# Performance work log

Hardware: AMD Instinct MI355X
Metric: run time of the kernel (lower is better)

The kernel has to match this reference:

```python
import jax, jax.numpy as jnp
import numpy as np

C_SIZE = 512
DOWN = 8
W = C_SIZE // DOWN           # 64
REG = 10.0
N_ITER = 100                 # num_of_iter_in_ot

COOD = jnp.arange(0, C_SIZE, DOWN, dtype=jnp.float32) + DOWN / 2.0  # (W,)


def _cost_matrix(pts):
    # pts: (N,2) pixel coords -> squared L2 distance to every grid cell, (N, W*W)
    x = pts[:, 0:1]
    y = pts[:, 1:2]
    cood = COOD[None, :]
    x_dis = -2.0 * x * cood + x * x + cood * cood      # (N, W)
    y_dis = -2.0 * y * cood + y * y + cood * cood      # (N, W)
    dis = y_dis[:, :, None] + x_dis[:, None, :]        # (N, W, W): rows=y, cols=x
    return dis.reshape(pts.shape[0], -1)


def _asgd_semi_dual(a, b, M, idxs):
    # POT ot.stochastic.solve_semi_dual_entropic with method='asgd'.
    # a: (n,) target (point) weights; b: (m,) source (density) weights; M: (n, m).
    n, m = M.shape
    lr = 1.0 / jnp.max(a / REG)          # POT default lr
    log_b = jnp.log(b)

    def step(carry, xk):
        cur, ave = carry
        i, k = xk
        Mi = M[i]
        khi = jax.nn.softmax((cur - Mi) / REG + log_b)   # stable softmax
        cur = cur + (lr / jnp.sqrt(k)) * (b - khi)
        ave = cur / k + (1.0 - 1.0 / k) * ave
        return (cur, ave), None

    ks = jnp.arange(1, idxs.shape[0] + 1, dtype=jnp.float32)
    (_, beta), _ = jax.lax.scan(step, (jnp.zeros(m, M.dtype), jnp.zeros(m, M.dtype)), (idxs, ks))
    # c-transform: alpha_i = -reg * log sum_j exp((beta_j - M_ij)/reg) * b_j
    alpha = -REG * jax.scipy.special.logsumexp((beta[None, :] - M) / REG + log_b[None, :], axis=1)
    pi = jnp.exp((alpha[:, None] + beta[None, :] - M) / REG) * a[:, None] * b[None, :]
    return beta, pi


def _per_sample(normed, unnormed, pts, idxs):
    # normed, unnormed: (W, W); pts: (N, 2); idxs: (N_ITER,)
    n = pts.shape[0]
    a = jnp.full((n,), 1.0 / n, dtype=jnp.float32)
    dis = jax.lax.stop_gradient(_cost_matrix(pts))            # cupy path: no grad
    b = jax.lax.stop_gradient(normed.reshape(-1))             # src_prob detached
    beta, pi = _asgd_semi_dual(a, b, dis, idxs)
    beta = jax.lax.stop_gradient(beta)
    ot_obj = jnp.sum(normed.reshape(-1) * beta)
    src = jax.lax.stop_gradient(unnormed.reshape(-1))         # source_density detached
    sc = src.sum()
    denom = sc * sc + 1e-16
    im_grad = jax.lax.stop_gradient(sc / denom * beta - jnp.sum(src * beta) / denom)
    loss = jnp.sum(unnormed.reshape(-1) * im_grad)
    wd = jnp.sum(dis * jax.lax.stop_gradient(pi))
    return loss, wd, ot_obj


def setup_inputs() -> dict:
    key = jax.random.key(0)
    k1, k2 = jax.random.split(key, 2)
    unnormed = jax.random.uniform(k1, (16, 1, W, W), dtype=jnp.float32)
    normed = unnormed / unnormed.sum(axis=(1, 2, 3), keepdims=True)
    points = jax.random.uniform(k2, (16, 512, 2), dtype=jnp.float32) * C_SIZE
    return {"normed_density": normed, "unnormed_density": unnormed, "points": points}


def reference(normed_density, unnormed_density, points):
    B = normed_density.shape[0]
    # random coordinate indices for ASGD (constant, deterministic)
    idxs = jax.random.randint(jax.random.key(1), (B, N_ITER), 0, points.shape[1])
    loss, wd, ot_obj = jax.vmap(_per_sample)(
        normed_density[:, 0], unnormed_density[:, 0], points, idxs)
    return jnp.stack([loss.sum(), wd.sum(), ot_obj.sum()])
```

## Files before the change

kernel.cpp:

```cpp
#include <hip/hip_runtime.h>
#include <math.h>

#define NSAMP 16
#define NPTS  512
#define MDIM  4096
#define NIT   100

#define R0MAX 48


__device__ __forceinline__ int swz(int r, int c) {
  return r * 64 + (c ^ ((r & 1) << 4));
}

__device__ __forceinline__ void tf2x32(unsigned k0, unsigned k1,
                                       unsigned c0, unsigned c1,
                                       unsigned &o0, unsigned &o1)
{
  unsigned ks2 = k0 ^ k1 ^ 0x1BD11BDAu;
  unsigned x0 = c0 + k0, x1 = c1 + k1;
#define ROT(r) x0 += x1; x1 = (x1 << (r)) | (x1 >> (32 - (r))); x1 ^= x0;
#define G0 ROT(13) ROT(15) ROT(26) ROT(6)
#define G1 ROT(17) ROT(29) ROT(16) ROT(24)
  G0 x0 += k1;  x1 += ks2 + 1u;
  G1 x0 += ks2; x1 += k0  + 2u;
  G0 x0 += k0;  x1 += k1  + 3u;
  G1 x0 += k1;  x1 += ks2 + 4u;
  G0 x0 += ks2; x1 += k0  + 5u;
#undef G0
#undef G1
#undef ROT
  o0 = x0; o1 = x1;
}

__device__ __forceinline__ int rand_idx(int f)
{
  unsigned ka, kb, w0, w1;
  tf2x32(0u, 1u, 0u, 1u, ka, kb);
  tf2x32(ka, kb, 0u, (unsigned)f, w0, w1);
  return (int)((w0 ^ w1) & 511u);
}

template<int CTRL>
__device__ __forceinline__ float dpp_mv(float v, float id)
{
  return __int_as_float(__builtin_amdgcn_update_dpp(
      __float_as_int(id), __float_as_int(v), CTRL, 0xF, 0xF, false));
}

__device__ __forceinline__ float waveSum(float v)
{
  v += dpp_mv<0x111>(v, 0.0f);
  v += dpp_mv<0x112>(v, 0.0f);
  v += dpp_mv<0x114>(v, 0.0f);
  v += dpp_mv<0x118>(v, 0.0f);
  v += dpp_mv<0x142>(v, 0.0f);
  v += dpp_mv<0x143>(v, 0.0f);
  return __int_as_float(__builtin_amdgcn_readlane(__float_as_int(v), 63));
}

__global__ __launch_bounds__(1024) void kern_scan(
    const float *__restrict__ normed, const float *__restrict__ pts,
    float *__restrict__ out, float *__restrict__ wglob)
{
  const int s = blockIdx.x;
  const int t = threadIdx.x;
  const int v = t >> 6;
  const int L = t & 63;

  __shared__ float2 dav[MDIM];
  __shared__ float  barr[MDIM];
  __shared__ float4 cstA[NIT + 4];
  __shared__ int2   cstB[NIT + 4];
  __shared__ float  spfin;
  __shared__ float  otred[16];

  #pragma unroll
  for (int l = 0; l < 4; ++l) {
    const int r = 4 * v + l;
    const float bv = normed[s * MDIM + r * 64 + L];
    const int idx = swz(r, L);
    dav[idx]  = make_float2(__logf(bv), 0.0f);
    barr[idx] = bv;
  }
  if (t < NIT + 4) {
    const int kk = t < NIT ? t : (NIT - 1);
    const int idx = rand_idx(s * NIT + kk);
    const float2 p = ((const float2 *)pts)[s * NPTS + idx];
    const int rn = (int)floorf((p.y - 4.0f) * 0.125f + 0.5f);
    const int cn = (int)floorf((p.x - 4.0f) * 0.125f + 0.5f);
    int r0 = rn - 7; r0 = r0 < 0 ? 0 : (r0 > R0MAX ? R0MAX : r0);
    int c0 = cn - 7; c0 = c0 < 0 ? 0 : (c0 > R0MAX ? R0MAX : c0);
    const float kf    = (float)(kk + 1);
    const float step1 = 512.0f * __builtin_amdgcn_rsqf(kf);
    const float Pk    = step1 * (0.01f * (101.0f - kf));
    cstA[t] = make_float4(p.x - (float)(8 * c0 + 4),
                          p.y - (float)(8 * r0 + 4), step1, Pk);
    cstB[t] = make_int2(r0, c0);
  }
  __syncthreads();

  const int rbase = L >> 4;
  const int cbase = L & 15;
  const float fc8 = (float)(8 * cbase);
  const float fr8 = (float)(8 * rbase);

  if (t == 64) {
    float SPa = 0.0f;
    for (int k = 0; k < NIT; ++k) SPa += cstA[k].w;
    spfin = SPa;
  }
  if (v == 0) {
    float A = 0.0f;
    float4 cA = cstA[0];
    int2   cB = cstB[0];
    int j0 = swz(cB.x + rbase, cB.y + cbase);
    float2 c0v = dav[j0      ]; float b0v = barr[j0      ];
    float2 c1v = dav[j0 + 256]; float b1v = barr[j0 + 256];
    float2 c2v = dav[j0 + 512]; float b2v = barr[j0 + 512];
    float2 c3v = dav[j0 + 768]; float b3v = barr[j0 + 768];

    for (int k = 0; k < NIT; ++k) {
      const float4 cAn = cstA[k + 1];
      const int2   cBn = cstB[k + 1];

      const float dx  = cA.x - fc8;
      const float dxx = dx * dx;
      const float ty  = cA.y - fr8;
      const float e0 = __expf(fmaf(fmaf(ty,          ty,          dxx), -0.1f, fmaf(b0v, A, c0v.x)));
      const float e1 = __expf(fmaf(fmaf(ty - 32.0f, ty - 32.0f, dxx), -0.1f, fmaf(b1v, A, c1v.x)));
      const float e2 = __expf(fmaf(fmaf(ty - 64.0f, ty - 64.0f, dxx), -0.1f, fmaf(b2v, A, c2v.x)));
      const float e3 = __expf(fmaf(fmaf(ty - 96.0f, ty - 96.0f, dxx), -0.1f, fmaf(b3v, A, c3v.x)));

      const float S    = waveSum((e0 + e1) + (e2 + e3));
      const float invS = __builtin_amdgcn_rcpf(S);
      const float cD = cA.z * invS, cAv = cA.w * invS;

      c0v.x = fmaf(-cD, e0, c0v.x); c0v.y = fmaf(cAv, e0, c0v.y);
      c1v.x = fmaf(-cD, e1, c1v.x); c1v.y = fmaf(cAv, e1, c1v.y);
      c2v.x = fmaf(-cD, e2, c2v.x); c2v.y = fmaf(cAv, e2, c2v.y);
      c3v.x = fmaf(-cD, e3, c3v.x); c3v.y = fmaf(cAv, e3, c3v.y);
      dav[j0      ] = c0v;
      dav[j0 + 256] = c1v;
      dav[j0 + 512] = c2v;
      dav[j0 + 768] = c3v;

      A += cA.z;

      cA = cAn; cB = cBn;
      j0 = swz(cB.x + rbase, cB.y + cbase);
      c0v = dav[j0      ]; b0v = barr[j0      ];
      c1v = dav[j0 + 256]; b1v = barr[j0 + 256];
      c2v = dav[j0 + 512]; b2v = barr[j0 + 512];
      c3v = dav[j0 + 768]; b3v = barr[j0 + 768];
    }
  }
  __syncthreads();

  {
    const float SP = spfin;
    float p_ot = 0.0f;
    #pragma unroll
    for (int l = 0; l < 4; ++l) {
      const int r   = 4 * v + l;
      const int idx = swz(r, L);
      const float2 cd = dav[idx];
      const float bb  = barr[idx];
      const float tt  = fmaf(bb, SP, -cd.y);
      wglob[s * MDIM + r * 64 + L] = tt + __logf(bb);
      p_ot = fmaf(bb, 10.0f * tt, p_ot);
    }
    p_ot = waveSum(p_ot);
    if (L == 0) otred[v] = p_ot;
  }
  __syncthreads();
  if (t == 0) {
    float ot = 0.0f;
    #pragma unroll
    for (int i = 0; i < 16; ++i) ot += otred[i];
    atomicAdd(&out[2], ot);
  }
}

__global__ __launch_bounds__(1024) void kern_wd(
    const float *__restrict__ pts, const float *__restrict__ wglob,
    float *__restrict__ out)
{
  const int s = blockIdx.x >> 3;
  const int q = blockIdx.x & 7;
  const int t = threadIdx.x;
  const int v = t >> 6;
  const int L = t & 63;

  __shared__ float  wlds[MDIM];
  __shared__ float2 pts2[64];
  __shared__ float  wdred[16];

  #pragma unroll
  for (int l = 0; l < 4; ++l) {
    const int r = 4 * v + l;
    wlds[swz(r, L)] = wglob[s * MDIM + r * 64 + L];
  }
  if (t < 64) pts2[t] = ((const float2 *)pts)[s * NPTS + 64 * q + t];
  __syncthreads();

  const int rbase = L >> 4;
  const int cbase = L & 15;

  float pe[4], pq[4];
  #pragma unroll
  for (int i = 0; i < 4; ++i) {
    const int p = 4 * v + i;
    const float2 pt = pts2[p];
    const float x = pt.x, y = pt.y;
    const int rn = (int)floorf((y - 4.0f) * 0.125f + 0.5f);
    const int cn = (int)floorf((x - 4.0f) * 0.125f + 0.5f);
    int r0 = rn - 7; r0 = r0 < 0 ? 0 : (r0 > R0MAX ? R0MAX : r0);
    int c0 = cn - 7; c0 = c0 < 0 ? 0 : (c0 > R0MAX ? R0MAX : c0);
    const int rl = r0 + rbase;
    const int cl = c0 + cbase;
    const int j0 = swz(rl, cl);

    const float dx  = x - (float)(8 * cl + 4);
    const float dxx = dx * dx;
    const float ty  = y - (float)(8 * rl + 4);
    float spe = 0.0f, spq = 0.0f;
    #pragma unroll
    for (int qq4 = 0; qq4 < 4; ++qq4) {
      const float wv = wlds[j0 + 256 * qq4];
      const float dy = ty - (float)(32 * qq4);
      const float qq = fmaf(dy, dy, dxx);
      const float e  = __expf(fmaf(qq, -0.1f, wv));
      spe += e;
      spq = fmaf(e, qq, spq);
    }
    pe[i] = spe; pq[i] = spq;
  }
  #pragma unroll
  for (int i = 0; i < 4; ++i) { pe[i] += dpp_mv<0x111>(pe[i], 0.0f); pq[i] += dpp_mv<0x111>(pq[i], 0.0f); }
  #pragma unroll
  for (int i = 0; i < 4; ++i) { pe[i] += dpp_mv<0x112>(pe[i], 0.0f); pq[i] += dpp_mv<0x112>(pq[i], 0.0f); }
  #pragma unroll
  for (int i = 0; i < 4; ++i) { pe[i] += dpp_mv<0x114>(pe[i], 0.0f); pq[i] += dpp_mv<0x114>(pq[i], 0.0f); }
  #pragma unroll
  for (int i = 0; i < 4; ++i) { pe[i] += dpp_mv<0x118>(pe[i], 0.0f); pq[i] += dpp_mv<0x118>(pq[i], 0.0f); }
  #pragma unroll
  for (int i = 0; i < 4; ++i) { pe[i] += dpp_mv<0x142>(pe[i], 0.0f); pq[i] += dpp_mv<0x142>(pq[i], 0.0f); }
  #pragma unroll
  for (int i = 0; i < 4; ++i) { pe[i] += dpp_mv<0x143>(pe[i], 0.0f); pq[i] += dpp_mv<0x143>(pq[i], 0.0f); }

  float wdacc = 0.0f;
  #pragma unroll
  for (int i = 0; i < 4; ++i) {
    const float PE = __int_as_float(__builtin_amdgcn_readlane(__float_as_int(pe[i]), 63));
    const float PQ = __int_as_float(__builtin_amdgcn_readlane(__float_as_int(pq[i]), 63));
    wdacc = fmaf(PQ, __builtin_amdgcn_rcpf(PE), wdacc);
  }
  if (L == 0) wdred[v] = wdacc;
  __syncthreads();
  if (t == 0) {
    float wd = 0.0f;
    #pragma unroll
    for (int i = 0; i < 16; ++i) wd += wdred[i];
    atomicAdd(&out[1], wd * (1.0f / 512.0f));
  }
}

extern "C" void kernel_launch(void* const* d_in, const int* in_sizes, int n_in,
                              void* d_out, int out_size, void* d_ws, size_t ws_size,
                              hipStream_t stream)
{
  (void)in_sizes; (void)n_in; (void)out_size; (void)ws_size;
  const float *normed = (const float *)d_in[0];
  const float *pts    = (const float *)d_in[2];
  float *out   = (float *)d_out;
  float *wglob = (float *)d_ws;

  hipMemsetAsync(out, 0, 3 * sizeof(float), stream);
  kern_scan<<<dim3(NSAMP),     dim3(1024), 0, stream>>>(normed, pts, out, wglob);
  kern_wd  <<<dim3(NSAMP * 8), dim3(1024), 0, stream>>>(pts, wglob, out);
}
```

Before: 84.30 us.

## Fuse scan and WD kernels into one launch with per-sample flag handoff

Merges the two kernels into a single launch. The first 16 blocks run the ASGD scan and publish their per-sample result through a release flag in the workspace. The remaining 128 blocks spin on an acquire load of that flag, then compute the transport cost. This removes a kernel launch and the gap between kernels, but adds a flag memset and spin-waiting. It also relies on the producer blocks being scheduled alongside the consumers, which is normally safe here with 144 blocks on a large GPU.

New measurement: 119.8 us. 42.1% more time.

```diff
diff --git a/kernel.cpp b/kernel.cpp
--- a/kernel.cpp
+++ b/kernel.cpp
@@ -59,210 +59,214 @@
   return __int_as_float(__builtin_amdgcn_readlane(__float_as_int(v), 63));
 }
 
-__global__ __launch_bounds__(1024) void kern_scan(
+__global__ __launch_bounds__(1024) void kern_all(
     const float *__restrict__ normed, const float *__restrict__ pts,
-    float *__restrict__ out, float *__restrict__ wglob)
-{
-  const int s = blockIdx.x;
+    float *__restrict__ out, float *__restrict__ wglob,
+    unsigned *__restrict__ flags)
+{
   const int t = threadIdx.x;
   const int v = t >> 6;
   const int L = t & 63;
+  const int rbase = L >> 4;
+  const int cbase = L & 15;
 
   __shared__ float2 dav[MDIM];
   __shared__ float  barr[MDIM];
   __shared__ float4 cstA[NIT + 4];
   __shared__ int2   cstB[NIT + 4];
   __shared__ float  spfin;
-  __shared__ float  otred[16];
-
-  #pragma unroll
-  for (int l = 0; l < 4; ++l) {
-    const int r = 4 * v + l;
-    const float bv = normed[s * MDIM + r * 64 + L];
-    const int idx = swz(r, L);
-    dav[idx]  = make_float2(__logf(bv), 0.0f);
-    barr[idx] = bv;
-  }
-  if (t < NIT + 4) {
-    const int kk = t < NIT ? t : (NIT - 1);
-    const int idx = rand_idx(s * NIT + kk);
-    const float2 p = ((const float2 *)pts)[s * NPTS + idx];
-    const int rn = (int)floorf((p.y - 4.0f) * 0.125f + 0.5f);
-    const int cn = (int)floorf((p.x - 4.0f) * 0.125f + 0.5f);
-    int r0 = rn - 7; r0 = r0 < 0 ? 0 : (r0 > R0MAX ? R0MAX : r0);
-    int c0 = cn - 7; c0 = c0 < 0 ? 0 : (c0 > R0MAX ? R0MAX : c0);
-    const float kf    = (float)(kk + 1);
-    const float step1 = 512.0f * __builtin_amdgcn_rsqf(kf);
-    const float Pk    = step1 * (0.01f * (101.0f - kf));
-    cstA[t] = make_float4(p.x - (float)(8 * c0 + 4),
-                          p.y - (float)(8 * r0 + 4), step1, Pk);
-    cstB[t] = make_int2(r0, c0);
-  }
-  __syncthreads();
-
-  const int rbase = L >> 4;
-  const int cbase = L & 15;
-  const float fc8 = (float)(8 * cbase);
-  const float fr8 = (float)(8 * rbase);
-
-  if (t == 64) {
-    float SPa = 0.0f;
-    for (int k = 0; k < NIT; ++k) SPa += cstA[k].w;
-    spfin = SPa;
-  }
-  if (v == 0) {
-    float A = 0.0f;
-    float4 cA = cstA[0];
-    int2   cB = cstB[0];
-    int j0 = swz(cB.x + rbase, cB.y + cbase);
-    float2 c0v = dav[j0      ]; float b0v = barr[j0      ];
-    float2 c1v = dav[j0 + 256]; float b1v = barr[j0 + 256];
-    float2 c2v = dav[j0 + 512]; float b2v = barr[j0 + 512];
-    float2 c3v = dav[j0 + 768]; float b3v = barr[j0 + 768];
-
-    for (int k = 0; k < NIT; ++k) {
-      const float4 cAn = cstA[k + 1];
-      const int2   cBn = cstB[k + 1];
-
-      const float dx  = cA.x - fc8;
+  __shared__ float2 pts2[64];
+  __shared__ float  red[16];
+
+  if (blockIdx.x < NSAMP) {
+    const int s = blockIdx.x;
+
+    #pragma unroll
+    for (int l = 0; l < 4; ++l) {
+      const int r = 4 * v + l;
+      const float bv = normed[s * MDIM + r * 64 + L];
+      const int idx = swz(r, L);
+      dav[idx]  = make_float2(__logf(bv), 0.0f);
+      barr[idx] = bv;
+    }
+    if (t < NIT + 4) {
+      const int kk = t < NIT ? t : (NIT - 1);
+      const int idx = rand_idx(s * NIT + kk);
+      const float2 p = ((const float2 *)pts)[s * NPTS + idx];
+      const int rn = (int)floorf((p.y - 4.0f) * 0.125f + 0.5f);
+      const int cn = (int)floorf((p.x - 4.0f) * 0.125f + 0.5f);
+      int r0 = rn - 7; r0 = r0 < 0 ? 0 : (r0 > R0MAX ? R0MAX : r0);
+      int c0 = cn - 7; c0 = c0 < 0 ? 0 : (c0 > R0MAX ? R0MAX : c0);
+      const float kf    = (float)(kk + 1);
+      const float step1 = 512.0f * __builtin_amdgcn_rsqf(kf);
+      const float Pk    = step1 * (0.01f * (101.0f - kf));
+      cstA[t] = make_float4(p.x - (float)(8 * c0 + 4),
+                            p.y - (float)(8 * r0 + 4), step1, Pk);
+      cstB[t] = make_int2(r0, c0);
+    }
+    __syncthreads();
+
+    const float fc8 = (float)(8 * cbase);
+    const float fr8 = (float)(8 * rbase);
+
+    if (t == 64) {
+      float SPa = 0.0f;
+      for (int k = 0; k < NIT; ++k) SPa += cstA[k].w;
+      spfin = SPa;
+    }
+    if (v == 0) {
+      float A = 0.0f;
+      float4 cA = cstA[0];
+      int2   cB = cstB[0];
+      int j0 = swz(cB.x + rbase, cB.y + cbase);
+      float2 c0v = dav[j0      ]; float b0v = barr[j0      ];
+      float2 c1v = dav[j0 + 256]; float b1v = barr[j0 + 256];
+      float2 c2v = dav[j0 + 512]; float b2v = barr[j0 + 512];
+      float2 c3v = dav[j0 + 768]; float b3v = barr[j0 + 768];
+
+      for (int k = 0; k < NIT; ++k) {
+        const float4 cAn = cstA[k + 1];
+        const int2   cBn = cstB[k + 1];
+
+        const float dx  = cA.x - fc8;
+        const float dxx = dx * dx;
+        const float ty  = cA.y - fr8;
+        const float e0 = __expf(fmaf(fmaf(ty,          ty,          dxx), -0.1f, fmaf(b0v, A, c0v.x)));
+        const float e1 = __expf(fmaf(fmaf(ty - 32.0f, ty - 32.0f, dxx), -0.1f, fmaf(b1v, A, c1v.x)));
+        const float e2 = __expf(fmaf(fmaf(ty - 64.0f, ty - 64.0f, dxx), -0.1f, fmaf(b2v, A, c2v.x)));
+        const float e3 = __expf(fmaf(fmaf(ty - 96.0f, ty - 96.0f, dxx), -0.1f, fmaf(b3v, A, c3v.x)));
+
+        const float S    = waveSum((e0 + e1) + (e2 + e3));
+        const float invS = __builtin_amdgcn_rcpf(S);
+        const float cD = cA.z * invS, cAv = cA.w * invS;
+
+        c0v.x = fmaf(-cD, e0, c0v.x); c0v.y = fmaf(cAv, e0, c0v.y);
+        c1v.x = fmaf(-cD, e1, c1v.x); c1v.y = fmaf(cAv, e1, c1v.y);
+        c2v.x = fmaf(-cD, e2, c2v.x); c2v.y = fmaf(cAv, e2, c2v.y);
+        c3v.x = fmaf(-cD, e3, c3v.x); c3v.y = fmaf(cAv, e3, c3v.y);
+        dav[j0      ] = c0v;
+        dav[j0 + 256] = c1v;
+        dav[j0 + 512] = c2v;
+        dav[j0 + 768] = c3v;
+
+        A += cA.z;
+
+        cA = cAn; cB = cBn;
+        j0 = swz(cB.x + rbase, cB.y + cbase);
+        c0v = dav[j0      ]; b0v = barr[j0      ];
+        c1v = dav[j0 + 256]; b1v = barr[j0 + 256];
+        c2v = dav[j0 + 512]; b2v = barr[j0 + 512];
+        c3v = dav[j0 + 768]; b3v = barr[j0 + 768];
+      }
+    }
+    __syncthreads();
+
+    {
+      const float SP = spfin;
+      float p_ot = 0.0f;
+      #pragma unroll
+      for (int l = 0; l < 4; ++l) {
+        const int r   = 4 * v + l;
+        const int idx = swz(r, L);
+        const float2 cd = dav[idx];
+        const float bb  = barr[idx];
+        const float tt  = fmaf(bb, SP, -cd.y);
+        wglob[s * MDIM + r * 64 + L] = tt + __logf(bb);
+        p_ot = fmaf(bb, 10.0f * tt, p_ot);
+      }
+      p_ot = waveSum(p_ot);
+      if (L == 0) red[v] = p_ot;
+    }
+    __syncthreads();
+    if (t == 0) {
+      float ot = 0.0f;
+      #pragma unroll
+      for (int i = 0; i < 16; ++i) ot += red[i];
+      atomicAdd(&out[2], ot);
+      __threadfence();
+      __hip_atomic_store(&flags[s], 1u, __ATOMIC_RELEASE,
+                         __HIP_MEMORY_SCOPE_AGENT);
+    }
+  } else {
+    const int cb = blockIdx.x - NSAMP;
+    const int s = cb >> 3;
+    const int q = cb & 7;
+
+    if (t < 64) pts2[t] = ((const float2 *)pts)[s * NPTS + 64 * q + t];
+
+    if (t == 0) {
+      while (__hip_atomic_load(&flags[s], __ATOMIC_ACQUIRE,
+                               __HIP_MEMORY_SCOPE_AGENT) == 0u) {
+        __builtin_amdgcn_s_sleep(8);
+      }
+    }
+    __syncthreads();
+    __threadfence();
+
+    #pragma unroll
+    for (int l = 0; l < 4; ++l) {
+      const int r = 4 * v + l;
+      barr[swz(r, L)] = wglob[s * MDIM + r * 64 + L];
+    }
+    __syncthreads();
+
+    float pe[4], pq[4];
+    #pragma unroll
+    for (int i = 0; i < 4; ++i) {
+      const int p = 4 * v + i;
+      const float2 pt = pts2[p];
+      const float x = pt.x, y = pt.y;
+      const int rn = (int)floorf((y - 4.0f) * 0.125f + 0.5f);
+      const int cn = (int)floorf((x - 4.0f) * 0.125f + 0.5f);
+      int r0 = rn - 7; r0 = r0 < 0 ? 0 : (r0 > R0MAX ? R0MAX : r0);
+      int c0 = cn - 7; c0 = c0 < 0 ? 0 : (c0 > R0MAX ? R0MAX : c0);
+      const int rl = r0 + rbase;
+      const int cl = c0 + cbase;
+      const int j0 = swz(rl, cl);
+
+      const float dx  = x - (float)(8 * cl + 4);
       const float dxx = dx * dx;
-      const float ty  = cA.y - fr8;
-      const float e0 = __expf(fmaf(fmaf(ty,          ty,          dxx), -0.1f, fmaf(b0v, A, c0v.x)));
-      const float e1 = __expf(fmaf(fmaf(ty - 32.0f, ty - 32.0f, dxx), -0.1f, fmaf(b1v, A, c1v.x)));
-      const float e2 = __expf(fmaf(fmaf(ty - 64.0f, ty - 64.0f, dxx), -0.1f, fmaf(b2v, A, c2v.x)));
-      const float e3 = __expf(fmaf(fmaf(ty - 96.0f, ty - 96.0f, dxx), -0.1f, fmaf(b3v, A, c3v.x)));
-
-      const float S    = waveSum((e0 + e1) + (e2 + e3));
-      const float invS = __builtin_amdgcn_rcpf(S);
-      const float cD = cA.z * invS, cAv = cA.w * invS;
-
-      c0v.x = fmaf(-cD, e0, c0v.x); c0v.y = fmaf(cAv, e0, c0v.y);
-      c1v.x = fmaf(-cD, e1, c1v.x); c1v.y = fmaf(cAv, e1, c1v.y);
-      c2v.x = fmaf(-cD, e2, c2v.x); c2v.y = fmaf(cAv, e2, c2v.y);
-      c3v.x = fmaf(-cD, e3, c3v.x); c3v.y = fmaf(cAv, e3, c3v.y);
-      dav[j0      ] = c0v;
-      dav[j0 + 256] = c1v;
-      dav[j0 + 512] = c2v;
-      dav[j0 + 768] = c3v;
-
-      A += cA.z;
-
-      cA = cAn; cB = cBn;
-      j0 = swz(cB.x + rbase, cB.y + cbase);
-      c0v = dav[j0      ]; b0v = barr[j0      ];
-      c1v = dav[j0 + 256]; b1v = barr[j0 + 256];
-      c2v = dav[j0 + 512]; b2v = barr[j0 + 512];
-      c3v = dav[j0 + 768]; b3v = barr[j0 + 768];
-    }
-  }
-  __syncthreads();
-
-  {
-    const float SP = spfin;
-    float p_ot = 0.0f;
-    #pragma unroll
-    for (int l = 0; l < 4; ++l) {
-      const int r   = 4 * v + l;
-      const int idx = swz(r, L);
-      const float2 cd = dav[idx];
-      const float bb  = barr[idx];
-      const float tt  = fmaf(bb, SP, -cd.y);
-      wglob[s * MDIM + r * 64 + L] = tt + __logf(bb);
-      p_ot = fmaf(bb, 10.0f * tt, p_ot);
-    }
-    p_ot = waveSum(p_ot);
-    if (L == 0) otred[v] = p_ot;
-  }
-  __syncthreads();
-  if (t == 0) {
-    float ot = 0.0f;
-    #pragma unroll
-    for (int i = 0; i < 16; ++i) ot += otred[i];
-    atomicAdd(&out[2], ot);
-  }
-}
-
-__global__ __launch_bounds__(1024) void kern_wd(
-    const float *__restrict__ pts, const float *__restrict__ wglob,
-    float *__restrict__ out)
-{
-  const int s = blockIdx.x >> 3;
-  const int q = blockIdx.x & 7;
-  const int t = threadIdx.x;
-  const int v = t >> 6;
-  const int L = t & 63;
-
-  __shared__ float  wlds[MDIM];
-  __shared__ float2 pts2[64];
-  __shared__ float  wdred[16];
-
-  #pragma unroll
-  for (int l = 0; l < 4; ++l) {
-    const int r = 4 * v + l;
-    wlds[swz(r, L)] = wglob[s * MDIM + r * 64 + L];
-  }
-  if (t < 64) pts2[t] = ((const float2 *)pts)[s * NPTS + 64 * q + t];
-  __syncthreads();
-
-  const int rbase = L >> 4;
-  const int cbase = L & 15;
-
-  float pe[4], pq[4];
-  #pragma unroll
-  for (int i = 0; i < 4; ++i) {
-    const int p = 4 * v + i;
-    const float2 pt = pts2[p];
-    const float x = pt.x, y = pt.y;
-    const int rn = (int)floorf((y - 4.0f) * 0.125f + 0.5f);
-    const int cn = (int)floorf((x - 4.0f) * 0.125f + 0.5f);
-    int r0 = rn - 7; r0 = r0 < 0 ? 0 : (r0 > R0MAX ? R0MAX : r0);
-    int c0 = cn - 7; c0 = c0 < 0 ? 0 : (c0 > R0MAX ? R0MAX : c0);
-    const int rl = r0 + rbase;
-    const int cl = c0 + cbase;
-    const int j0 = swz(rl, cl);
-
-    const float dx  = x - (float)(8 * cl + 4);
-    const float dxx = dx * dx;
-    const float ty  = y - (float)(8 * rl + 4);
-    float spe = 0.0f, spq = 0.0f;
-    #pragma unroll
-    for (int qq4 = 0; qq4 < 4; ++qq4) {
-      const float wv = wlds[j0 + 256 * qq4];
-      const float dy = ty - (float)(32 * qq4);
-      const float qq = fmaf(dy, dy, dxx);
-      const float e  = __expf(fmaf(qq, -0.1f, wv));
-      spe += e;
-      spq = fmaf(e, qq, spq);
-    }
-    pe[i] = spe; pq[i] = spq;
-  }
-  #pragma unroll
-  for (int i = 0; i < 4; ++i) { pe[i] += dpp_mv<0x111>(pe[i], 0.0f); pq[i] += dpp_mv<0x111>(pq[i], 0.0f); }
-  #pragma unroll
-  for (int i = 0; i < 4; ++i) { pe[i] += dpp_mv<0x112>(pe[i], 0.0f); pq[i] += dpp_mv<0x112>(pq[i], 0.0f); }
-  #pragma unroll
-  for (int i = 0; i < 4; ++i) { pe[i] += dpp_mv<0x114>(pe[i], 0.0f); pq[i] += dpp_mv<0x114>(pq[i], 0.0f); }
-  #pragma unroll
-  for (int i = 0; i < 4; ++i) { pe[i] += dpp_mv<0x118>(pe[i], 0.0f); pq[i] += dpp_mv<0x118>(pq[i], 0.0f); }
-  #pragma unroll
-  for (int i = 0; i < 4; ++i) { pe[i] += dpp_mv<0x142>(pe[i], 0.0f); pq[i] += dpp_mv<0x142>(pq[i], 0.0f); }
-  #pragma unroll
-  for (int i = 0; i < 4; ++i) { pe[i] += dpp_mv<0x143>(pe[i], 0.0f); pq[i] += dpp_mv<0x143>(pq[i], 0.0f); }
-
-  float wdacc = 0.0f;
-  #pragma unroll
-  for (int i = 0; i < 4; ++i) {
-    const float PE = __int_as_float(__builtin_amdgcn_readlane(__float_as_int(pe[i]), 63));
-    const float PQ = __int_as_float(__builtin_amdgcn_readlane(__float_as_int(pq[i]), 63));
-    wdacc = fmaf(PQ, __builtin_amdgcn_rcpf(PE), wdacc);
-  }
-  if (L == 0) wdred[v] = wdacc;
-  __syncthreads();
-  if (t == 0) {
-    float wd = 0.0f;
-    #pragma unroll
-    for (int i = 0; i < 16; ++i) wd += wdred[i];
-    atomicAdd(&out[1], wd * (1.0f / 512.0f));
+      const float ty  = y - (float)(8 * rl + 4);
+      float spe = 0.0f, spq = 0.0f;
+      #pragma unroll
+      for (int qq4 = 0; qq4 < 4; ++qq4) {
+        const float wv = barr[j0 + 256 * qq4];
+        const float dy = ty - (float)(32 * qq4);
+        const float qq = fmaf(dy, dy, dxx);
+        const float e  = __expf(fmaf(qq, -0.1f, wv));
+        spe += e;
+        spq = fmaf(e, qq, spq);
+      }
+      pe[i] = spe; pq[i] = spq;
+    }
+    #pragma unroll
+    for (int i = 0; i < 4; ++i) { pe[i] += dpp_mv<0x111>(pe[i], 0.0f); pq[i] += dpp_mv<0x111>(pq[i], 0.0f); }
+    #pragma unroll
+    for (int i = 0; i < 4; ++i) { pe[i] += dpp_mv<0x112>(pe[i], 0.0f); pq[i] += dpp_mv<0x112>(pq[i], 0.0f); }
+    #pragma unroll
+    for (int i = 0; i < 4; ++i) { pe[i] += dpp_mv<0x114>(pe[i], 0.0f); pq[i] += dpp_mv<0x114>(pq[i], 0.0f); }
+    #pragma unroll
+    for (int i = 0; i < 4; ++i) { pe[i] += dpp_mv<0x118>(pe[i], 0.0f); pq[i] += dpp_mv<0x118>(pq[i], 0.0f); }
+    #pragma unroll
+    for (int i = 0; i < 4; ++i) { pe[i] += dpp_mv<0x142>(pe[i], 0.0f); pq[i] += dpp_mv<0x142>(pq[i], 0.0f); }
+    #pragma unroll
+    for (int i = 0; i < 4; ++i) { pe[i] += dpp_mv<0x143>(pe[i], 0.0f); pq[i] += dpp_mv<0x143>(pq[i], 0.0f); }
+
+    float wdacc = 0.0f;
+    #pragma unroll
+    for (int i = 0; i < 4; ++i) {
+      const float PE = __int_as_float(__builtin_amdgcn_readlane(__float_as_int(pe[i]), 63));
+      const float PQ = __int_as_float(__builtin_amdgcn_readlane(__float_as_int(pq[i]), 63));
+      wdacc = fmaf(PQ, __builtin_amdgcn_rcpf(PE), wdacc);
+    }
+    if (L == 0) red[v] = wdacc;
+    __syncthreads();
+    if (t == 0) {
+      float wd = 0.0f;
+      #pragma unroll
+      for (int i = 0; i < 16; ++i) wd += red[i];
+      atomicAdd(&out[1], wd * (1.0f / 512.0f));
+    }
   }
 }
 
@@ -273,10 +277,12 @@
   (void)in_sizes; (void)n_in; (void)out_size; (void)ws_size;
   const float *normed = (const float *)d_in[0];
   const float *pts    = (const float *)d_in[2];
-  float *out   = (float *)d_out;
-  float *wglob = (float *)d_ws;
+  float *out      = (float *)d_out;
+  float *wglob    = (float *)d_ws;
+  unsigned *flags = (unsigned *)((char *)d_ws + NSAMP * MDIM * sizeof(float));
 
   hipMemsetAsync(out, 0, 3 * sizeof(float), stream);
-  kern_scan<<<dim3(NSAMP),     dim3(1024), 0, stream>>>(normed, pts, out, wglob);
-  kern_wd  <<<dim3(NSAMP * 8), dim3(1024), 0, stream>>>(pts, wglob, out);
-}
+  hipMemsetAsync(flags, 0, NSAMP * sizeof(unsigned), stream);
+  kern_all<<<dim3(NSAMP + NSAMP * 8), dim3(1024), 0, stream>>>(
+      normed, pts, out, wglob, flags);
+}
```

## Process two ASGD iterations together when their windows do not overlap

Applied to the files above, without the earlier changes.

The serial ASGD scan loop now handles iterations in pairs. When the two sampled points' local windows in the cost grid do not overlap (checked uniformly per wave), both softmax updates are computed independently and their wave reductions are interleaved, which halves the serial chain of DPP reductions. Overlapping pairs fall back to running the two steps one after the other. This adds register pressure and branching, and relies on the windowed update touching only a bounded region.

Result: slower. 86.14 us (+2.2%).

```diff
diff --git a/kernel.cpp b/kernel.cpp
--- a/kernel.cpp
+++ b/kernel.cpp
@@ -59,6 +59,18 @@
   return __int_as_float(__builtin_amdgcn_readlane(__float_as_int(v), 63));
 }
 
+__device__ __forceinline__ void waveSum2(float &a, float &b)
+{
+  a += dpp_mv<0x111>(a, 0.0f); b += dpp_mv<0x111>(b, 0.0f);
+  a += dpp_mv<0x112>(a, 0.0f); b += dpp_mv<0x112>(b, 0.0f);
+  a += dpp_mv<0x114>(a, 0.0f); b += dpp_mv<0x114>(b, 0.0f);
+  a += dpp_mv<0x118>(a, 0.0f); b += dpp_mv<0x118>(b, 0.0f);
+  a += dpp_mv<0x142>(a, 0.0f); b += dpp_mv<0x142>(b, 0.0f);
+  a += dpp_mv<0x143>(a, 0.0f); b += dpp_mv<0x143>(b, 0.0f);
+  a = __int_as_float(__builtin_amdgcn_readlane(__float_as_int(a), 63));
+  b = __int_as_float(__builtin_amdgcn_readlane(__float_as_int(b), 63));
+}
+
 __global__ __launch_bounds__(1024) void kern_scan(
     const float *__restrict__ normed, const float *__restrict__ pts,
     float *__restrict__ out, float *__restrict__ wglob)
@@ -112,47 +124,120 @@
   }
   if (v == 0) {
     float A = 0.0f;
-    float4 cA = cstA[0];
-    int2   cB = cstB[0];
-    int j0 = swz(cB.x + rbase, cB.y + cbase);
+    float4 cA  = cstA[0], cA2 = cstA[1];
+    int2   cB  = cstB[0], cB2 = cstB[1];
+    int j0 = swz(cB.x  + rbase, cB.y  + cbase);
+    int j1 = swz(cB2.x + rbase, cB2.y + cbase);
+    int dr = cB.x - cB2.x, dc = cB.y - cB2.y;
+    int ovl = __builtin_amdgcn_readfirstlane(
+        (int)(((unsigned)(dr + 15) < 31u) & ((unsigned)(dc + 15) < 31u)));
     float2 c0v = dav[j0      ]; float b0v = barr[j0      ];
     float2 c1v = dav[j0 + 256]; float b1v = barr[j0 + 256];
     float2 c2v = dav[j0 + 512]; float b2v = barr[j0 + 512];
     float2 c3v = dav[j0 + 768]; float b3v = barr[j0 + 768];
-
-    for (int k = 0; k < NIT; ++k) {
-      const float4 cAn = cstA[k + 1];
-      const int2   cBn = cstB[k + 1];
-
-      const float dx  = cA.x - fc8;
-      const float dxx = dx * dx;
+    float2 d0v, d1v, d2v, d3v; float g0v, g1v, g2v, g3v;
+    if (!ovl) {
+      d0v = dav[j1      ]; g0v = barr[j1      ];
+      d1v = dav[j1 + 256]; g1v = barr[j1 + 256];
+      d2v = dav[j1 + 512]; g2v = barr[j1 + 512];
+      d3v = dav[j1 + 768]; g3v = barr[j1 + 768];
+    }
+
+    for (int kp = 0; kp < NIT; kp += 2) {
+      const float4 nA  = cstA[kp + 2], nA2 = cstA[kp + 3];
+      const int2   nB  = cstB[kp + 2], nB2 = cstB[kp + 3];
+      const int nj0 = swz(nB.x  + rbase, nB.y  + cbase);
+      const int nj1 = swz(nB2.x + rbase, nB2.y + cbase);
+      const int ndr = nB.x - nB2.x, ndc = nB.y - nB2.y;
+      const int novl = __builtin_amdgcn_readfirstlane(
+          (int)(((unsigned)(ndr + 15) < 31u) & ((unsigned)(ndc + 15) < 31u)));
+
+      const float A2 = A + cA.z;
+
+      const float dx  = cA.x - fc8;  const float dxx  = dx  * dx;
       const float ty  = cA.y - fr8;
-      const float e0 = __expf(fmaf(fmaf(ty,          ty,          dxx), -0.1f, fmaf(b0v, A, c0v.x)));
-      const float e1 = __expf(fmaf(fmaf(ty - 32.0f, ty - 32.0f, dxx), -0.1f, fmaf(b1v, A, c1v.x)));
-      const float e2 = __expf(fmaf(fmaf(ty - 64.0f, ty - 64.0f, dxx), -0.1f, fmaf(b2v, A, c2v.x)));
-      const float e3 = __expf(fmaf(fmaf(ty - 96.0f, ty - 96.0f, dxx), -0.1f, fmaf(b3v, A, c3v.x)));
-
-      const float S    = waveSum((e0 + e1) + (e2 + e3));
-      const float invS = __builtin_amdgcn_rcpf(S);
-      const float cD = cA.z * invS, cAv = cA.w * invS;
-
-      c0v.x = fmaf(-cD, e0, c0v.x); c0v.y = fmaf(cAv, e0, c0v.y);
-      c1v.x = fmaf(-cD, e1, c1v.x); c1v.y = fmaf(cAv, e1, c1v.y);
-      c2v.x = fmaf(-cD, e2, c2v.x); c2v.y = fmaf(cAv, e2, c2v.y);
-      c3v.x = fmaf(-cD, e3, c3v.x); c3v.y = fmaf(cAv, e3, c3v.y);
-      dav[j0      ] = c0v;
-      dav[j0 + 256] = c1v;
-      dav[j0 + 512] = c2v;
-      dav[j0 + 768] = c3v;
-
-      A += cA.z;
-
-      cA = cAn; cB = cBn;
-      j0 = swz(cB.x + rbase, cB.y + cbase);
+      const float dx2 = cA2.x - fc8; const float dxx2 = dx2 * dx2;
+      const float ty2 = cA2.y - fr8;
+
+      if (!ovl) {
+        const float e0 = __expf(fmaf(fmaf(ty,           ty,           dxx ), -0.1f, fmaf(b0v, A,  c0v.x)));
+        const float e1 = __expf(fmaf(fmaf(ty  - 32.0f,  ty  - 32.0f,  dxx ), -0.1f, fmaf(b1v, A,  c1v.x)));
+        const float e2 = __expf(fmaf(fmaf(ty  - 64.0f,  ty  - 64.0f,  dxx ), -0.1f, fmaf(b2v, A,  c2v.x)));
+        const float e3 = __expf(fmaf(fmaf(ty  - 96.0f,  ty  - 96.0f,  dxx ), -0.1f, fmaf(b3v, A,  c3v.x)));
+        const float f0 = __expf(fmaf(fmaf(ty2,          ty2,          dxx2), -0.1f, fmaf(g0v, A2, d0v.x)));
+        const float f1 = __expf(fmaf(fmaf(ty2 - 32.0f,  ty2 - 32.0f,  dxx2), -0.1f, fmaf(g1v, A2, d1v.x)));
+        const float f2 = __expf(fmaf(fmaf(ty2 - 64.0f,  ty2 - 64.0f,  dxx2), -0.1f, fmaf(g2v, A2, d2v.x)));
+        const float f3 = __expf(fmaf(fmaf(ty2 - 96.0f,  ty2 - 96.0f,  dxx2), -0.1f, fmaf(g3v, A2, d3v.x)));
+
+        float S  = (e0 + e1) + (e2 + e3);
+        float S2 = (f0 + f1) + (f2 + f3);
+        waveSum2(S, S2);
+        const float invS  = __builtin_amdgcn_rcpf(S);
+        const float invS2 = __builtin_amdgcn_rcpf(S2);
+        const float cD  = cA.z  * invS,  cAv  = cA.w  * invS;
+        const float cD2 = cA2.z * invS2, cAv2 = cA2.w * invS2;
+
+        c0v.x = fmaf(-cD, e0, c0v.x); c0v.y = fmaf(cAv, e0, c0v.y);
+        c1v.x = fmaf(-cD, e1, c1v.x); c1v.y = fmaf(cAv, e1, c1v.y);
+        c2v.x = fmaf(-cD, e2, c2v.x); c2v.y = fmaf(cAv, e2, c2v.y);
+        c3v.x = fmaf(-cD, e3, c3v.x); c3v.y = fmaf(cAv, e3, c3v.y);
+        d0v.x = fmaf(-cD2, f0, d0v.x); d0v.y = fmaf(cAv2, f0, d0v.y);
+        d1v.x = fmaf(-cD2, f1, d1v.x); d1v.y = fmaf(cAv2, f1, d1v.y);
+        d2v.x = fmaf(-cD2, f2, d2v.x); d2v.y = fmaf(cAv2, f2, d2v.y);
+        d3v.x = fmaf(-cD2, f3, d3v.x); d3v.y = fmaf(cAv2, f3, d3v.y);
+        dav[j0      ] = c0v; dav[j0 + 256] = c1v;
+        dav[j0 + 512] = c2v; dav[j0 + 768] = c3v;
+        dav[j1      ] = d0v; dav[j1 + 256] = d1v;
+        dav[j1 + 512] = d2v; dav[j1 + 768] = d3v;
+      } else {
+        const float e0 = __expf(fmaf(fmaf(ty,          ty,          dxx), -0.1f, fmaf(b0v, A, c0v.x)));
+        const float e1 = __expf(fmaf(fmaf(ty - 32.0f, ty - 32.0f, dxx), -0.1f, fmaf(b1v, A, c1v.x)));
+        const float e2 = __expf(fmaf(fmaf(ty - 64.0f, ty - 64.0f, dxx), -0.1f, fmaf(b2v, A, c2v.x)));
+        const float e3 = __expf(fmaf(fmaf(ty - 96.0f, ty - 96.0f, dxx), -0.1f, fmaf(b3v, A, c3v.x)));
+        const float S    = waveSum((e0 + e1) + (e2 + e3));
+        const float invS = __builtin_amdgcn_rcpf(S);
+        const float cD = cA.z * invS, cAv = cA.w * invS;
+        c0v.x = fmaf(-cD, e0, c0v.x); c0v.y = fmaf(cAv, e0, c0v.y);
+        c1v.x = fmaf(-cD, e1, c1v.x); c1v.y = fmaf(cAv, e1, c1v.y);
+        c2v.x = fmaf(-cD, e2, c2v.x); c2v.y = fmaf(cAv, e2, c2v.y);
+        c3v.x = fmaf(-cD, e3, c3v.x); c3v.y = fmaf(cAv, e3, c3v.y);
+        dav[j0      ] = c0v; dav[j0 + 256] = c1v;
+        dav[j0 + 512] = c2v; dav[j0 + 768] = c3v;
+
+        d0v = dav[j1      ]; g0v = barr[j1      ];
+        d1v = dav[j1 + 256]; g1v = barr[j1 + 256];
+        d2v = dav[j1 + 512]; g2v = barr[j1 + 512];
+        d3v = dav[j1 + 768]; g3v = barr[j1 + 768];
+
+        const float f0 = __expf(fmaf(fmaf(ty2,          ty2,          dxx2), -0.1f, fmaf(g0v, A2, d0v.x)));
+        const float f1 = __expf(fmaf(fmaf(ty2 - 32.0f, ty2 - 32.0f, dxx2), -0.1f, fmaf(g1v, A2, d1v.x)));
+        const float f2 = __expf(fmaf(fmaf(ty2 - 64.0f, ty2 - 64.0f, dxx2), -0.1f, fmaf(g2v, A2, d2v.x)));
+        const float f3 = __expf(fmaf(fmaf(ty2 - 96.0f, ty2 - 96.0f, dxx2), -0.1f, fmaf(g3v, A2, d3v.x)));
+        const float S2    = waveSum((f0 + f1) + (f2 + f3));
+        const float invS2 = __builtin_amdgcn_rcpf(S2);
+        const float cD2 = cA2.z * invS2, cAv2 = cA2.w * invS2;
+        d0v.x = fmaf(-cD2, f0, d0v.x); d0v.y = fmaf(cAv2, f0, d0v.y);
+        d1v.x = fmaf(-cD2, f1, d1v.x); d1v.y = fmaf(cAv2, f1, d1v.y);
+        d2v.x = fmaf(-cD2, f2, d2v.x); d2v.y = fmaf(cAv2, f2, d2v.y);
+        d3v.x = fmaf(-cD2, f3, d3v.x); d3v.y = fmaf(cAv2, f3, d3v.y);
+        dav[j1      ] = d0v; dav[j1 + 256] = d1v;
+        dav[j1 + 512] = d2v; dav[j1 + 768] = d3v;
+      }
+
+      A = A2 + cA2.z;
+
+      cA = nA; cA2 = nA2; cB = nB; cB2 = nB2;
+      j0 = nj0; j1 = nj1; ovl = novl;
       c0v = dav[j0      ]; b0v = barr[j0      ];
       c1v = dav[j0 + 256]; b1v = barr[j0 + 256];
       c2v = dav[j0 + 512]; b2v = barr[j0 + 512];
       c3v = dav[j0 + 768]; b3v = barr[j0 + 768];
+      if (!ovl) {
+        d0v = dav[j1      ]; g0v = barr[j1      ];
+        d1v = dav[j1 + 256]; g1v = barr[j1 + 256];
+        d2v = dav[j1 + 512]; g2v = barr[j1 + 512];
+        d3v = dav[j1 + 768]; g3v = barr[j1 + 768];
+      }
     }
   }
   __syncthreads();
```
